# Optimization experiments

Measured on AMD Instinct MI355X. Metric: run time of the kernel, lower is better.

Reference implementation:

```python
import jax, jax.numpy as jnp
import numpy as np

N, E, B, D = 50000, 800000, 250, 128
EPS = 1e-5


def setup_inputs() -> dict:
    key = jax.random.key(0)
    ks = jax.random.split(key, 12)
    x = jax.random.normal(ks[0], (N, D), jnp.float32)
    w = jax.random.uniform(ks[1], (E, 4), jnp.float32)
    src = jax.random.randint(ks[2], (E,), 0, N)
    dst = jax.random.randint(ks[3], (E,), 0, N)
    graph_ids = jnp.sort(jax.random.randint(ks[4], (N,), 0, B))
    s = 1.0 / np.sqrt(D)
    W1 = jax.random.normal(ks[5], (D, D), jnp.float32) * s
    W2 = jax.random.normal(ks[6], (D, D), jnp.float32) * s
    W3 = jax.random.normal(ks[7], (D, D), jnp.float32) * s
    ln1_g = jnp.ones((D,), jnp.float32)
    ln1_b = jnp.zeros((D,), jnp.float32)
    ln2_g = jnp.ones((D,), jnp.float32)
    ln2_b = jnp.zeros((D,), jnp.float32)
    return dict(x=x, w=w, W1=W1, W2=W2, W3=W3, ln1_g=ln1_g, ln1_b=ln1_b,
                ln2_g=ln2_g, ln2_b=ln2_b, src=src, dst=dst, graph_ids=graph_ids)


def _layernorm(h, g, b):
    mu = jnp.mean(h, axis=-1, keepdims=True)
    var = jnp.mean(jnp.square(h - mu), axis=-1, keepdims=True)
    return (h - mu) * jax.lax.rsqrt(var + EPS) * g + b


def reference(x, w, W1, W2, W3, ln1_g, ln1_b, ln2_g, ln2_b, src, dst, graph_ids):
    # edge feature [E,Fe] -> scalar edge weight [E] (mean over feature dim)
    w_s = jnp.mean(w, axis=-1)
    ones_e = jnp.ones((E,), x.dtype)
    # DGL norm='both': unweighted degrees, clamped to >= 1
    out_deg = jnp.clip(jax.ops.segment_sum(ones_e, src, num_segments=N), 1.0)
    in_deg = jnp.clip(jax.ops.segment_sum(ones_e, dst, num_segments=N), 1.0)
    out_norm = jax.lax.rsqrt(out_deg)[:, None]  # [N,1]
    in_norm = jax.lax.rsqrt(in_deg)[:, None]    # [N,1]

    def gconv(h, W):
        m = (h * out_norm)[src] * w_s[:, None]                 # [E,D] gather-mul
        agg = jax.ops.segment_sum(m, dst, num_segments=N)      # [N,D] scatter-add
        return (agg * in_norm) @ W                              # [N,D_out]

    h = _layernorm(jax.nn.relu(gconv(x, W1)), ln1_g, ln1_b)
    h = _layernorm(jax.nn.relu(gconv(h, W2)), ln2_g, ln2_b)
    h = gconv(h, W3)
    # per-graph segmented sum readout -> [B, D]
    return jax.ops.segment_sum(h, graph_ids, num_segments=B)
```

## Files before the change

kernel.cpp:

```cpp
#include <hip/hip_runtime.h>

#define D 128
#define RS 16
#define NBMAX 1024
constexpr float EPS = 1e-5f;

typedef short bf16x8 __attribute__((ext_vector_type(8)));
typedef float f32x4 __attribute__((ext_vector_type(4)));
typedef unsigned long long u64;

__device__ __forceinline__ uint f2bf(float f) {
  union { float f; uint u; } v; v.f = f;
  return (v.u + 0x7fffu + ((v.u >> 16) & 1u)) >> 16;
}
__device__ __forceinline__ float bflo(uint u) {
  union { uint u; float f; } v; v.u = u << 16; return v.f;
}
__device__ __forceinline__ float bfhi(uint u) {
  union { uint u; float f; } v; v.u = u & 0xffff0000u; return v.f;
}

__device__ __forceinline__ int lower_bound(const int* __restrict__ a, int n, int key) {
  int lo = 0, hi = n;
  while (lo < hi) { int m = (lo + hi) >> 1; if (a[m] < key) lo = m + 1; else hi = m; }
  return lo;
}

__global__ __launch_bounds__(256) void k_pre(
    const int* __restrict__ src, const int* __restrict__ dst,
    int* __restrict__ btot, int* __restrict__ btot2, int E, int nb, int ebA,
    const float4* __restrict__ x, uint4* __restrict__ xb, int n8, int cb,
    const float* __restrict__ W1, const float* __restrict__ W2,
    const float* __restrict__ W3, ushort* __restrict__ Wf) {
  __shared__ int hd[NBMAX];
  __shared__ int hs[NBMAX];
  int bid = blockIdx.x;
  int tid = threadIdx.x;
  if (bid < ebA) {
    for (int j = tid; j < nb; j += 256) { hd[j] = 0; hs[j] = 0; }
    __syncthreads();
    int e0 = bid * 4096;
#pragma unroll 4
    for (int it = 0; it < 16; ++it) {
      int e = e0 + it * 256 + tid;
      if (e < E) {
        atomicAdd(&hd[dst[e] >> 6], 1);
        atomicAdd(&hs[src[e] >> 6], 1);
      }
    }
    __syncthreads();
    for (int j = tid; j < nb; j += 256) {
      int cd = hd[j];
      if (cd) atomicAdd(&btot[j], cd);
      int cs = hs[j];
      if (cs) atomicAdd(&btot2[j], cs);
    }
  } else if (bid < ebA + cb) {
    int i = (bid - ebA) * 256 + tid;
    if (i < n8) {
      float4 p = x[i * 2], q = x[i * 2 + 1];
      uint4 o;
      o.x = f2bf(p.x) | (f2bf(p.y) << 16);
      o.y = f2bf(p.z) | (f2bf(p.w) << 16);
      o.z = f2bf(q.x) | (f2bf(q.y) << 16);
      o.w = f2bf(q.z) | (f2bf(q.w) << 16);
      xb[i] = o;
    }
  } else {
    int t4 = (bid - ebA - cb) * 256 + tid;
    if (t4 < 3 * 2048) {
      const float* Wsrc = (t4 < 2048) ? W1 : (t4 < 4096) ? W2 : W3;
      int t = t4 & 2047;
      int lane = t & 63;
      int frag = t >> 6;
      int ks = frag >> 3, ct = frag & 7;
      int col = ct * 16 + (lane & 15);
      int kb = ks * 32 + (lane >> 4) * 8;
      uint p[8];
#pragma unroll
      for (int j = 0; j < 8; ++j) p[j] = f2bf(Wsrc[(kb + j) * D + col]);
      uint4 o;
      o.x = p[0] | (p[1] << 16);
      o.y = p[2] | (p[3] << 16);
      o.z = p[4] | (p[5] << 16);
      o.w = p[6] | (p[7] << 16);
      *(uint4*)(Wf + (size_t)t4 * 8) = o;
    }
  }
}

__global__ __launch_bounds__(1024) void k_bbase(
    const int* __restrict__ btot, const int* __restrict__ btot2,
    int* __restrict__ bb, int* __restrict__ bb2,
    int* __restrict__ rowptr, int nb, int E, int N) {
  __shared__ int part[1024];
  int t = threadIdx.x;
  int v = (t < nb) ? btot[t] : 0;
  part[t] = v;
  __syncthreads();
  for (int off = 1; off < 1024; off <<= 1) {
    int u = (t >= off) ? part[t - off] : 0;
    __syncthreads();
    part[t] += u;
    __syncthreads();
  }
  if (t < nb) bb[t] = part[t] - v;
  if (t == 0) { bb[nb] = E; rowptr[N] = E; }
  __syncthreads();
  int v2 = (t < nb) ? btot2[t] : 0;
  part[t] = v2;
  __syncthreads();
  for (int off = 1; off < 1024; off <<= 1) {
    int u = (t >= off) ? part[t - off] : 0;
    __syncthreads();
    part[t] += u;
    __syncthreads();
  }
  if (t < nb) bb2[t] = part[t] - v2;
  if (t == 0) bb2[nb] = E;
}

__global__ __launch_bounds__(256) void k_bscatter(
    const int* __restrict__ src, const int* __restrict__ dst,
    const float4* __restrict__ w,
    const int* __restrict__ bb, int* __restrict__ bcur,
    const int* __restrict__ bb2, int* __restrict__ bcur2,
    u64* __restrict__ ebuf, uint* __restrict__ ebuf2, int E, int nb) {
  __shared__ int hd[NBMAX], hdc[NBMAX];
  __shared__ int hsv[NBMAX], hsc[NBMAX];
  int bid = blockIdx.x, tid = threadIdx.x;
  for (int j = tid; j < nb; j += 256) { hd[j] = 0; hsv[j] = 0; }
  __syncthreads();
  int e0 = bid * 4096;
#pragma unroll 4
  for (int it = 0; it < 16; ++it) {
    int e = e0 + it * 256 + tid;
    if (e < E) {
      atomicAdd(&hd[dst[e] >> 6], 1);
      atomicAdd(&hsv[src[e] >> 6], 1);
    }
  }
  __syncthreads();
  for (int j = tid; j < nb; j += 256) {
    int cd = hd[j];
    hdc[j] = cd ? (bb[j] + atomicAdd(&bcur[j], cd)) : 0;
    int cs = hsv[j];
    hsc[j] = cs ? (bb2[j] + atomicAdd(&bcur2[j], cs)) : 0;
  }
  __syncthreads();
#pragma unroll 4
  for (int it = 0; it < 16; ++it) {
    int e = e0 + it * 256 + tid;
    if (e < E) {
      int d = dst[e], s = src[e];
      int pos = atomicAdd(&hdc[d >> 6], 1);
      float4 wv = w[e];
      float meanw = (wv.x + wv.y + wv.z + wv.w) * 0.25f;
      u64 pk = ((u64)__float_as_uint(meanw) << 32) |
               ((u64)(d & 63) << 16) | (uint)s;
      ebuf[pos] = pk;
      int pos2 = atomicAdd(&hsc[s >> 6], 1);
      ebuf2[pos2] = (uint)s;
    }
  }
}

__global__ __launch_bounds__(256) void k_scount(
    const uint* __restrict__ ebuf2, const int* __restrict__ bb2,
    float* __restrict__ outn, int N) {
  __shared__ int c64[64];
  int b = blockIdx.x, tid = threadIdx.x;
  int base = bb2[b];
  int cnt = bb2[b + 1] - base;
  if (tid < 64) c64[tid] = 0;
  __syncthreads();
  for (int i = tid; i < cnt; i += 256)
    atomicAdd(&c64[ebuf2[base + i] & 63], 1);
  __syncthreads();
  if (tid < 64) {
    int node = b * 64 + tid;
    if (node < N) outn[node] = rsqrtf(fmaxf((float)c64[tid], 1.0f));
  }
}

__global__ __launch_bounds__(256) void k_bplace(
    const u64* __restrict__ ebuf, const int* __restrict__ bb,
    const float* __restrict__ outn,
    int* __restrict__ rowptr, float* __restrict__ innm,
    u64* __restrict__ ecsr, int N) {
  __shared__ int c64[64], ex[64], cur[64];
  int b = blockIdx.x, tid = threadIdx.x;
  int base = bb[b];
  int cnt = bb[b + 1] - base;
  if (tid < 64) c64[tid] = 0;
  __syncthreads();
  for (int i = tid; i < cnt; i += 256) {
    u64 v = ebuf[base + i];
    atomicAdd(&c64[(int)((v >> 16) & 63)], 1);
  }
  __syncthreads();
  if (tid < 64) {
    int cv = c64[tid];
    int inc = cv;
#pragma unroll
    for (int off = 1; off < 64; off <<= 1) {
      int u = __shfl_up(inc, off);
      if (tid >= off) inc += u;
    }
    int excl = inc - cv;
    ex[tid] = excl;
    cur[tid] = 0;
    int node = b * 64 + tid;
    if (node < N) {
      rowptr[node] = base + excl;
      innm[node] = rsqrtf(fmaxf((float)cv, 1.0f));
    }
  }
  __syncthreads();
  for (int i = tid; i < cnt; i += 256) {
    u64 v = ebuf[base + i];
    int dl = (int)((v >> 16) & 63);
    int s = (int)(v & 0xFFFFu);
    float coef = __uint_as_float((uint)(v >> 32)) * outn[s];
    int pos = base + ex[dl] + atomicAdd(&cur[dl], 1);
    ecsr[pos] = ((u64)__float_as_uint(coef) << 32) | (uint)s;
  }
}

__global__ __launch_bounds__(256) void k_fused(
    const ushort* __restrict__ h, const int* __restrict__ rowptr,
    const u64* __restrict__ ecsr,
    const float* __restrict__ innm, const ushort* __restrict__ Wf,
    const float* __restrict__ g, const float* __restrict__ bta,
    void* __restrict__ out, int N, int do_ln) {
  __shared__ float lds[4][16 * D];
  const int lane = threadIdx.x & 63;
  const int wv = threadIdx.x >> 6;
  const int row0 = blockIdx.x * 64 + wv * 16;
  if (row0 >= N) return;

  ushort* at = (ushort*)&lds[wv][0];
  {
    const int grp = lane >> 4;
    const int c = lane & 15;
    for (int rr = 0; rr < 4; ++rr) {
      int n = row0 + grp * 4 + rr;
      if (n >= N) break;
      int beg = rowptr[n], end = rowptr[n + 1];
      float a0 = 0, a1 = 0, a2 = 0, a3 = 0, a4 = 0, a5 = 0, a6 = 0, a7 = 0;
#define ACC8(q, f)                                          \
  a0 = fmaf(bflo(q.x), f, a0); a1 = fmaf(bfhi(q.x), f, a1); \
  a2 = fmaf(bflo(q.y), f, a2); a3 = fmaf(bfhi(q.y), f, a3); \
  a4 = fmaf(bflo(q.z), f, a4); a5 = fmaf(bfhi(q.z), f, a5); \
  a6 = fmaf(bflo(q.w), f, a6); a7 = fmaf(bfhi(q.w), f, a7);
      int j = beg;
      for (; j + 4 <= end; j += 4) {
        u64 v0 = ecsr[j], v1 = ecsr[j + 1], v2 = ecsr[j + 2], v3 = ecsr[j + 3];
        const ushort* p0 = h + (size_t)(v0 & 0xFFFFu) * D + c * 8;
        const ushort* p1 = h + (size_t)(v1 & 0xFFFFu) * D + c * 8;
        const ushort* p2 = h + (size_t)(v2 & 0xFFFFu) * D + c * 8;
        const ushort* p3 = h + (size_t)(v3 & 0xFFFFu) * D + c * 8;
        float f0 = __uint_as_float((uint)(v0 >> 32));
        float f1 = __uint_as_float((uint)(v1 >> 32));
        float f2 = __uint_as_float((uint)(v2 >> 32));
        float f3 = __uint_as_float((uint)(v3 >> 32));
        uint4 q0 = *(const uint4*)p0;
        uint4 q1 = *(const uint4*)p1;
        uint4 q2 = *(const uint4*)p2;
        uint4 q3 = *(const uint4*)p3;
        ACC8(q0, f0) ACC8(q1, f1) ACC8(q2, f2) ACC8(q3, f3)
      }
      for (; j < end; ++j) {
        u64 v = ecsr[j];
        float f = __uint_as_float((uint)(v >> 32));
        uint4 q = *(const uint4*)(h + (size_t)(v & 0xFFFFu) * D + c * 8);
        ACC8(q, f)
      }
#undef ACC8
      float sc = innm[n];
      uint4 o;
      o.x = f2bf(a0 * sc) | (f2bf(a1 * sc) << 16);
      o.y = f2bf(a2 * sc) | (f2bf(a3 * sc) << 16);
      o.z = f2bf(a4 * sc) | (f2bf(a5 * sc) << 16);
      o.w = f2bf(a6 * sc) | (f2bf(a7 * sc) << 16);
      *(uint4*)(at + (grp * 4 + rr) * 136 + c * 8) = o;
    }
  }
  asm volatile("s_waitcnt lgkmcnt(0)" ::: "memory");
  __builtin_amdgcn_sched_barrier(0);

  const int lc = lane & 15, lg = lane >> 4;
  f32x4 acc[8];
#pragma unroll
  for (int ct = 0; ct < 8; ++ct) acc[ct] = (f32x4){0.f, 0.f, 0.f, 0.f};
#pragma unroll
  for (int ks = 0; ks < 4; ++ks) {
    bf16x8 a = *(const bf16x8*)(at + lc * 136 + ks * 32 + lg * 8);
    const ushort* wp = Wf + ((size_t)(ks * 8) * 64 + lane) * 8;
#pragma unroll
    for (int ct = 0; ct < 8; ++ct) {
      bf16x8 b = *(const bf16x8*)(wp + ct * 512);
      acc[ct] = __builtin_amdgcn_mfma_f32_16x16x32_bf16(a, b, acc[ct], 0, 0, 0);
    }
  }
  asm volatile("s_waitcnt lgkmcnt(0)" ::: "memory");
  __builtin_amdgcn_sched_barrier(0);

  if (do_ln) {
    float v[8][4];
#pragma unroll
    for (int ct = 0; ct < 8; ++ct)
#pragma unroll
      for (int j = 0; j < 4; ++j) v[ct][j] = fmaxf(acc[ct][j], 0.f);
    float mu[4], rs[4];
#pragma unroll
    for (int j = 0; j < 4; ++j) {
      float s = 0.f;
#pragma unroll
      for (int ct = 0; ct < 8; ++ct) s += v[ct][j];
#pragma unroll
      for (int off = 1; off < 16; off <<= 1) s += __shfl_xor(s, off);
      mu[j] = s * (1.0f / D);
    }
#pragma unroll
    for (int j = 0; j < 4; ++j) {
      float q = 0.f;
#pragma unroll
      for (int ct = 0; ct < 8; ++ct) {
        v[ct][j] -= mu[j];
        q = fmaf(v[ct][j], v[ct][j], q);
      }
#pragma unroll
      for (int off = 1; off < 16; off <<= 1) q += __shfl_xor(q, off);
      rs[j] = rsqrtf(q * (1.0f / D) + EPS);
    }
    ushort* lp = (ushort*)&lds[wv][0];
#pragma unroll
    for (int ct = 0; ct < 8; ++ct) {
      float gc = g[ct * 16 + lc], bc = bta[ct * 16 + lc];
#pragma unroll
      for (int j = 0; j < 4; ++j)
        lp[(lg * 4 + j) * D + ct * 16 + lc] = (ushort)f2bf(fmaf(v[ct][j] * rs[j], gc, bc));
    }
    __builtin_amdgcn_wave_barrier();
    int r = row0 + (lane >> 2);
    if (r < N) {
      ushort* ob = (ushort*)out + (size_t)row0 * D + lane * 32;
#pragma unroll
      for (int i = 0; i < 4; ++i)
        ((uint4*)ob)[i] = ((const uint4*)(lp + lane * 32))[i];
    }
  } else {
    float* lp = &lds[wv][0];
#pragma unroll
    for (int ct = 0; ct < 8; ++ct)
#pragma unroll
      for (int j = 0; j < 4; ++j)
        lp[(lg * 4 + j) * D + ct * 16 + lc] = acc[ct][j];
    __builtin_amdgcn_wave_barrier();
    int r = row0 + (lane >> 2);
    if (r < N) {
      float* ob = (float*)out + (size_t)row0 * D + lane * 32;
#pragma unroll
      for (int i = 0; i < 8; ++i)
        ((float4*)ob)[i] = ((const float4*)(lp + lane * 32))[i];
    }
  }
}

__global__ __launch_bounds__(128) void k_rpart(
    const float* __restrict__ h, const int* __restrict__ gid,
    float* __restrict__ part, int N) {
  int b = blockIdx.x / RS, s = blockIdx.x % RS;
  int t = threadIdx.x;
  int start = lower_bound(gid, N, b);
  int end = lower_bound(gid, N, b + 1);
  int len = end - start;
  int chunk = (len + RS - 1) / RS;
  int rb = start + s * chunk;
  int re = min(rb + chunk, end);
  float acc = 0.f;
  for (int n = rb; n < re; ++n) acc += h[(size_t)n * D + t];
  part[((size_t)b * RS + s) * D + t] = acc;
}

__global__ __launch_bounds__(128) void k_rsum(
    const float* __restrict__ part, float* __restrict__ out) {
  int b = blockIdx.x;
  int t = threadIdx.x;
  float acc = 0.f;
#pragma unroll
  for (int s = 0; s < RS; ++s) acc += part[((size_t)b * RS + s) * D + t];
  out[(size_t)b * D + t] = acc;
}

extern "C" void kernel_launch(void* const* d_in, const int* in_sizes, int n_in,
                              void* d_out, int out_size, void* d_ws, size_t ws_size,
                              hipStream_t stream) {
  const float* x    = (const float*)d_in[0];
  const float* w    = (const float*)d_in[1];
  const float* W1   = (const float*)d_in[2];
  const float* W2   = (const float*)d_in[3];
  const float* W3   = (const float*)d_in[4];
  const float* ln1g = (const float*)d_in[5];
  const float* ln1b = (const float*)d_in[6];
  const float* ln2g = (const float*)d_in[7];
  const float* ln2b = (const float*)d_in[8];
  const int* src = (const int*)d_in[9];
  const int* dst = (const int*)d_in[10];
  const int* gid = (const int*)d_in[11];
  const int N = in_sizes[0] / D;
  const int E = in_sizes[9];
  const int B = out_size / D;
  float* outp = (float*)d_out;

  float*  h3f  = (float*)d_ws;
  ushort* xb   = (ushort*)(h3f + (size_t)N * D);
  ushort* hb1  = xb + (size_t)N * D;
  ushort* Wf   = hb1 + (size_t)N * D;
  float*  outn = (float*)(Wf + 3 * 2048 * 8);
  float*  innm = outn + N;
  const int nb  = (N + 63) >> 6;
  const int ebA = (E + 4095) / 4096;
  int*    btot = (int*)(innm + N);
  int*    bcur = btot + nb;
  int*    btot2= bcur + nb;
  int*    bcur2= btot2 + nb;
  int*    rowptr = bcur2 + nb;
  int*    bb   = rowptr + N + 2;
  int*    bb2  = bb + nb + 2;
  u64*    ecsr = (u64*)(bb2 + nb + 2);
  float*  part = (float*)(ecsr + E);
  u64*    ebuf = (u64*)h3f;
  uint*   ebuf2= (uint*)(ebuf + E);

  const int mb  = (N + 63) / 64;
  const int n8  = N * D / 8;
  const int cb  = (n8 + 255) / 256;

  hipMemsetAsync(btot, 0, sizeof(int) * (size_t)(4 * nb), stream);
  k_pre<<<ebA + cb + 24, 256, 0, stream>>>(src, dst, btot, btot2, E, nb, ebA,
                                           (const float4*)x, (uint4*)xb, n8, cb,
                                           W1, W2, W3, Wf);
  k_bbase<<<1, 1024, 0, stream>>>(btot, btot2, bb, bb2, rowptr, nb, E, N);
  k_bscatter<<<ebA, 256, 0, stream>>>(src, dst, (const float4*)w, bb, bcur,
                                      bb2, bcur2, ebuf, ebuf2, E, nb);
  k_scount<<<nb, 256, 0, stream>>>(ebuf2, bb2, outn, N);
  k_bplace<<<nb, 256, 0, stream>>>(ebuf, bb, outn, rowptr, innm, ecsr, N);

  k_fused<<<mb, 256, 0, stream>>>(xb, rowptr, ecsr, innm, Wf,
                                  ln1g, ln1b, hb1, N, 1);
  k_fused<<<mb, 256, 0, stream>>>(hb1, rowptr, ecsr, innm, Wf + 16384,
                                  ln2g, ln2b, xb, N, 1);
  k_fused<<<mb, 256, 0, stream>>>(xb, rowptr, ecsr, innm, Wf + 32768,
                                  nullptr, nullptr, h3f, N, 0);

  k_rpart<<<B * RS, 128, 0, stream>>>(h3f, gid, part, N);
  k_rsum<<<B, 128, 0, stream>>>(part, outp);
}
```

Baseline: 212.4 us.

## Stage bucketed edges in LDS with local counting sort before coalesced global writes

The edge bucketing kernel now sorts each 4096-edge chunk by destination and source bucket in shared memory, using per-block prefix scans. It then writes the contiguous runs to the global bucket buffers, so the scattered global stores become mostly contiguous ones. The block size goes from 256 to 512 threads, and the packed edge word now carries the full destination index instead of its low 6 bits. In exchange, the kernel adds two block-wide scans with many barriers and a larger LDS footprint, which may reduce occupancy.

```diff
diff --git a/kernel.cpp b/kernel.cpp
--- a/kernel.cpp
+++ b/kernel.cpp
@@ -120,48 +120,91 @@
   if (t == 0) bb2[nb] = E;
 }
 
-__global__ __launch_bounds__(256) void k_bscatter(
+__global__ __launch_bounds__(512) void k_bscatter(
     const int* __restrict__ src, const int* __restrict__ dst,
     const float4* __restrict__ w,
     const int* __restrict__ bb, int* __restrict__ bcur,
     const int* __restrict__ bb2, int* __restrict__ bcur2,
     u64* __restrict__ ebuf, uint* __restrict__ ebuf2, int E, int nb) {
-  __shared__ int hd[NBMAX], hdc[NBMAX];
-  __shared__ int hsv[NBMAX], hsc[NBMAX];
+  __shared__ u64 sedge[4096];
+  __shared__ uint ssrc[4096];
+  __shared__ int hd[NBMAX], sd[NBMAX], dd[NBMAX];
+  __shared__ int hs[NBMAX], s2[NBMAX], d2[NBMAX];
+  __shared__ int psum[512];
   int bid = blockIdx.x, tid = threadIdx.x;
-  for (int j = tid; j < nb; j += 256) { hd[j] = 0; hsv[j] = 0; }
-  __syncthreads();
   int e0 = bid * 4096;
-#pragma unroll 4
-  for (int it = 0; it < 16; ++it) {
-    int e = e0 + it * 256 + tid;
-    if (e < E) {
-      atomicAdd(&hd[dst[e] >> 6], 1);
-      atomicAdd(&hsv[src[e] >> 6], 1);
-    }
-  }
-  __syncthreads();
-  for (int j = tid; j < nb; j += 256) {
+  int ec = min(4096, E - e0);
+  for (int j = tid; j < nb; j += 512) { hd[j] = 0; hs[j] = 0; }
+  __syncthreads();
+#pragma unroll
+  for (int it = 0; it < 8; ++it) {
+    int i = it * 512 + tid;
+    if (i < ec) {
+      atomicAdd(&hd[dst[e0 + i] >> 6], 1);
+      atomicAdd(&hs[src[e0 + i] >> 6], 1);
+    }
+  }
+  __syncthreads();
+  {
+    int a0 = (2 * tid < nb) ? hd[2 * tid] : 0;
+    int a1 = (2 * tid + 1 < nb) ? hd[2 * tid + 1] : 0;
+    int p = a0 + a1;
+    psum[tid] = p;
+    __syncthreads();
+    for (int off = 1; off < 512; off <<= 1) {
+      int u = (tid >= off) ? psum[tid - off] : 0;
+      __syncthreads();
+      psum[tid] += u;
+      __syncthreads();
+    }
+    int ex = psum[tid] - p;
+    if (2 * tid < nb) sd[2 * tid] = ex;
+    if (2 * tid + 1 < nb) sd[2 * tid + 1] = ex + a0;
+  }
+  __syncthreads();
+  {
+    int a0 = (2 * tid < nb) ? hs[2 * tid] : 0;
+    int a1 = (2 * tid + 1 < nb) ? hs[2 * tid + 1] : 0;
+    int p = a0 + a1;
+    psum[tid] = p;
+    __syncthreads();
+    for (int off = 1; off < 512; off <<= 1) {
+      int u = (tid >= off) ? psum[tid - off] : 0;
+      __syncthreads();
+      psum[tid] += u;
+      __syncthreads();
+    }
+    int ex = psum[tid] - p;
+    if (2 * tid < nb) s2[2 * tid] = ex;
+    if (2 * tid + 1 < nb) s2[2 * tid + 1] = ex + a0;
+  }
+  __syncthreads();
+  for (int j = tid; j < nb; j += 512) {
     int cd = hd[j];
-    hdc[j] = cd ? (bb[j] + atomicAdd(&bcur[j], cd)) : 0;
-    int cs = hsv[j];
-    hsc[j] = cs ? (bb2[j] + atomicAdd(&bcur2[j], cs)) : 0;
-  }
-  __syncthreads();
-#pragma unroll 4
-  for (int it = 0; it < 16; ++it) {
-    int e = e0 + it * 256 + tid;
-    if (e < E) {
-      int d = dst[e], s = src[e];
-      int pos = atomicAdd(&hdc[d >> 6], 1);
-      float4 wv = w[e];
+    dd[j] = cd ? (bb[j] + atomicAdd(&bcur[j], cd) - sd[j]) : 0;
+    int cs = hs[j];
+    d2[j] = cs ? (bb2[j] + atomicAdd(&bcur2[j], cs) - s2[j]) : 0;
+  }
+  __syncthreads();
+#pragma unroll
+  for (int it = 0; it < 8; ++it) {
+    int i = it * 512 + tid;
+    if (i < ec) {
+      int d = dst[e0 + i], s = src[e0 + i];
+      float4 wv = w[e0 + i];
       float meanw = (wv.x + wv.y + wv.z + wv.w) * 0.25f;
-      u64 pk = ((u64)__float_as_uint(meanw) << 32) |
-               ((u64)(d & 63) << 16) | (uint)s;
-      ebuf[pos] = pk;
-      int pos2 = atomicAdd(&hsc[s >> 6], 1);
-      ebuf2[pos2] = (uint)s;
-    }
+      u64 pk = ((u64)__float_as_uint(meanw) << 32) | ((u64)(uint)d << 16) | (uint)s;
+      sedge[atomicAdd(&sd[d >> 6], 1)] = pk;
+      ssrc[atomicAdd(&s2[s >> 6], 1)] = (uint)s;
+    }
+  }
+  __syncthreads();
+  for (int i = tid; i < ec; i += 512) {
+    u64 v = sedge[i];
+    int j = (int)((v >> 16) & 0xFFFFu) >> 6;
+    ebuf[dd[j] + i] = v;
+    uint s = ssrc[i];
+    ebuf2[d2[s >> 6] + i] = s;
   }
 }
 
@@ -443,7 +486,7 @@
                                            (const float4*)x, (uint4*)xb, n8, cb,
                                            W1, W2, W3, Wf);
   k_bbase<<<1, 1024, 0, stream>>>(btot, btot2, bb, bb2, rowptr, nb, E, N);
-  k_bscatter<<<ebA, 256, 0, stream>>>(src, dst, (const float4*)w, bb, bcur,
+  k_bscatter<<<ebA, 512, 0, stream>>>(src, dst, (const float4*)w, bb, bcur,
                                       bb2, bcur2, ebuf, ebuf2, E, nb);
   k_scount<<<nb, 256, 0, stream>>>(ebuf2, bb2, outn, N);
   k_bplace<<<nb, 256, 0, stream>>>(ebuf, bb, outn, rowptr, innm, ecsr, N);
```

New measurement: 203.8 us. -4.1%, faster.
